# Kernel optimization log

Hardware: AMD Instinct MI355X
Metric: run time of the kernel (lower is better)

The kernel has to match this reference:

```python
import jax, jax.numpy as jnp
import numpy as np

B, L, D = 1, 2048, 2048
H, KV, HD = 32, 8, 64
REP = H // KV  # GQA repeat factor = 4


def _rope(t, cos, sin):
    # t: (B, L, nH, HD); cos/sin: (L, HD//2). Complex rotation on (even, odd) pairs.
    tr = t.reshape(*t.shape[:-1], HD // 2, 2)
    xr, xi = tr[..., 0], tr[..., 1]
    c = cos[None, :, None, :]
    s = sin[None, :, None, :]
    out_r = xr * c - xi * s
    out_i = xr * s + xi * c
    return jnp.stack([out_r, out_i], axis=-1).reshape(t.shape)


def setup_inputs() -> dict:
    key = jax.random.key(0)
    ks = jax.random.split(key, 5)
    x = jax.random.normal(ks[0], (B, L, D), jnp.float32)
    wq = jax.random.normal(ks[1], (D, H * HD), jnp.float32) * 0.02
    wk = jax.random.normal(ks[2], (D, KV * HD), jnp.float32) * 0.02
    wv = jax.random.normal(ks[3], (D, KV * HD), jnp.float32) * 0.02
    wo = jax.random.normal(ks[4], (H * HD, D), jnp.float32) * 0.02
    pos = jnp.arange(L, dtype=jnp.float32)
    inv_freq = 1.0 / (10000.0 ** (jnp.arange(0, HD, 2, dtype=jnp.float32) / HD))
    ang = pos[:, None] * inv_freq[None, :]  # (L, HD//2)
    freqs_cos = jnp.cos(ang)
    freqs_sin = jnp.sin(ang)
    # causal additive mask (L, L): 0 on/below diagonal, large negative above
    causal = jnp.arange(L)[None, :] <= jnp.arange(L)[:, None]
    mask = jnp.where(causal, 0.0, -1e9).astype(jnp.float32)
    return {"x": x, "wq": wq, "wk": wk, "wv": wv, "wo": wo,
            "freqs_cos": freqs_cos, "freqs_sin": freqs_sin, "mask": mask}


def reference(x, wq, wk, wv, wo, freqs_cos, freqs_sin, mask):
    q = (x @ wq).reshape(B, L, H, HD)
    k = (x @ wk).reshape(B, L, KV, HD)
    v = (x @ wv).reshape(B, L, KV, HD)
    q = _rope(q, freqs_cos, freqs_sin)
    k = _rope(k, freqs_cos, freqs_sin)
    # GQA: repeat_interleave kv heads
    k = jnp.repeat(k, REP, axis=2)
    v = jnp.repeat(v, REP, axis=2)
    # (B, nH, L, HD)
    q = q.transpose(0, 2, 1, 3)
    k = k.transpose(0, 2, 1, 3)
    v = v.transpose(0, 2, 1, 3)
    scores = jnp.einsum('bhqd,bhkd->bhqk', q, k) / np.float32(np.sqrt(HD))
    scores = scores + mask[None, None, :, :]
    attn = jax.nn.softmax(scores.astype(jnp.float32), axis=-1).astype(q.dtype)
    out = jnp.einsum('bhqk,bhkd->bqhd', attn, v).reshape(B, L, H * HD)
    return out @ wo
```

## Files before the change

### kernel.cpp

```cpp
#include <hip/hip_runtime.h>
#include <hip/hip_bf16.h>

#define L 2048
#define D 2048
#define NH 32
#define NKV 8
#define HD 64

typedef unsigned short u16;
typedef __attribute__((ext_vector_type(8))) short bf16x8;
typedef __attribute__((ext_vector_type(4))) short bf16x4;
typedef __attribute__((ext_vector_type(4))) float f32x4;

#define QSCALE 0.1803368801f

__device__ __forceinline__ f32x4 mfma16(bf16x4 a, bf16x4 b, f32x4 c) {
    return __builtin_amdgcn_mfma_f32_16x16x16bf16_1k(a, b, c, 0, 0, 0);
}

#define PANEL_OFF(d0, k) ((((size_t)((d0) >> 7) * 64 + ((k) >> 5)) << 12) + (((d0) & 127) << 5) + ((k) & 31))

__device__ __forceinline__ u16 f2bf(float x) {
    __hip_bfloat16 b = __float2bfloat16(x);
    return *reinterpret_cast<u16*>(&b);
}

__device__ __forceinline__ void gload_lds16(const void* g, void* l) {
    __builtin_amdgcn_global_load_lds(
        (const __attribute__((address_space(1))) unsigned int*)g,
        (__attribute__((address_space(3))) unsigned int*)l, 16, 0, 0);
}

__global__ __launch_bounds__(256) void prep_kernel(
    const float* __restrict__ x, u16* __restrict__ xb,
    const float* __restrict__ wq, const float* __restrict__ wk,
    const float* __restrict__ wv, const float* __restrict__ wo,
    u16* __restrict__ wqkvT, u16* __restrict__ woT)
{
    const int z = blockIdx.z;
    if (z == 4) {
        int i = (blockIdx.y * 64 + blockIdx.x) * 256 + threadIdx.x;
        int e = i * 4;
        int row = e >> 11, k0 = e & 2047;
        float4 v = ((const float4*)x)[i];
        ushort4 o;
        o.x = f2bf(v.x); o.y = f2bf(v.y); o.z = f2bf(v.z); o.w = f2bf(v.w);
        *(ushort4*)&xb[PANEL_OFF(row, k0)] = o;
        return;
    }
    const float* src; u16* dst; int C;
    if (z == 0)      { src = wq; dst = wqkvT;                           C = 2048; }
    else if (z == 1) { src = wk; dst = wqkvT + (size_t)2048 * 2048;     C = 512;  }
    else if (z == 2) { src = wv; dst = wqkvT + (size_t)2560 * 2048;     C = 512;  }
    else             { src = wo; dst = woT;                             C = 2048; }
    const int c0 = blockIdx.x * 32;
    if (c0 >= C) return;
    const int r0 = blockIdx.y * 32;
    __shared__ float tile[32][33];
    const int tx = threadIdx.x & 31, ty = threadIdx.x >> 5;
#pragma unroll
    for (int i = 0; i < 32; i += 8)
        tile[ty + i][tx] = src[(size_t)(r0 + ty + i) * C + c0 + tx];
    __syncthreads();
#pragma unroll
    for (int i = 0; i < 32; i += 8) {
        const int n = c0 + ty + i, k = r0 + tx;
        dst[PANEL_OFF(n, k)] = f2bf(tile[tx][ty + i]);
    }
}

#define VT_LDS 72

template <int MODE>
__global__ __launch_bounds__(256) void gemm4w_kernel(
    const u16* __restrict__ A, const u16* __restrict__ Bt, void* __restrict__ Cout,
    int N, int K, const float* __restrict__ fc, const float* __restrict__ fs,
    u16* __restrict__ vt)
{
    __shared__ __align__(16) u16 As[4][128 * 32];
    __shared__ __align__(16) u16 Bs[4][128 * 32];
    const int tid = threadIdx.x;
    const int w = tid >> 6, lane = tid & 63;

    const int nwg = (int)(gridDim.x * gridDim.y);
    int bid = (int)blockIdx.y * (int)gridDim.x + (int)blockIdx.x;
    bid = (bid & 7) * (nwg >> 3) + (bid >> 3);
    const int m0 = (bid / (int)gridDim.x) * 128, n0 = (bid % (int)gridDim.x) * 128;

    const int l15 = lane & 15, quad = lane >> 4, q8 = quad * 8;
    const int wr = (w >> 1) * 64, wc = (w & 1) * 64;
    const int l8 = lane * 8;
    const int wch = w * 1024;

    const u16* pa = A  + ((size_t)(m0 >> 7) * (K / 32) << 12);
    const u16* pb = Bt + ((size_t)(n0 >> 7) * (K / 32) << 12);

    f32x4 acc[4][4];
#pragma unroll
    for (int i = 0; i < 4; ++i)
#pragma unroll
        for (int j = 0; j < 4; ++j) acc[i][j] = (f32x4){0.f, 0.f, 0.f, 0.f};

    const int nSub = K / 32;
    const int nOut = nSub / 2;
#pragma unroll
    for (int s = 0; s < 4; ++s) {
        const size_t so = (size_t)s << 12;
        gload_lds16(pa + so + wch + l8,       &As[s][wch]);
        gload_lds16(pa + so + wch + 512 + l8, &As[s][wch + 512]);
        gload_lds16(pb + so + wch + l8,       &Bs[s][wch]);
        gload_lds16(pb + so + wch + 512 + l8, &Bs[s][wch + 512]);
    }
    for (int it = 0; it < nOut; ++it) {
        const int s0 = 2 * it, cb0 = s0 & 3, cb1 = (s0 + 1) & 3;
        asm volatile("s_waitcnt vmcnt(8)" ::: "memory");
        asm volatile("s_barrier" ::: "memory");
        bf16x8 a0[4], a1[4], b0[4], b1[4];
#pragma unroll
        for (int t = 0; t < 4; ++t) {
            a0[t] = *(const bf16x8*)&As[cb0][(wr + t * 16 + l15) * 32 + q8];
            b0[t] = *(const bf16x8*)&Bs[cb0][(wc + t * 16 + l15) * 32 + q8];
            a1[t] = *(const bf16x8*)&As[cb1][(wr + t * 16 + l15) * 32 + q8];
            b1[t] = *(const bf16x8*)&Bs[cb1][(wc + t * 16 + l15) * 32 + q8];
        }
        asm volatile("s_waitcnt lgkmcnt(0)" ::: "memory");
        asm volatile("s_barrier" ::: "memory");
        {
            const int sp0 = s0 + 4, sp1 = s0 + 5;
            const size_t k0 = (size_t)((sp0 < nSub) ? sp0 : 0) << 12;
            const size_t k1 = (size_t)((sp1 < nSub) ? sp1 : 0) << 12;
            gload_lds16(pa + k0 + wch + l8,       &As[cb0][wch]);
            gload_lds16(pa + k0 + wch + 512 + l8, &As[cb0][wch + 512]);
            gload_lds16(pb + k0 + wch + l8,       &Bs[cb0][wch]);
            gload_lds16(pb + k0 + wch + 512 + l8, &Bs[cb0][wch + 512]);
            gload_lds16(pa + k1 + wch + l8,       &As[cb1][wch]);
            gload_lds16(pa + k1 + wch + 512 + l8, &As[cb1][wch + 512]);
            gload_lds16(pb + k1 + wch + l8,       &Bs[cb1][wch]);
            gload_lds16(pb + k1 + wch + 512 + l8, &Bs[cb1][wch + 512]);
        }
#pragma unroll
        for (int i = 0; i < 4; ++i)
#pragma unroll
            for (int j = 0; j < 4; ++j) {
                acc[i][j] = __builtin_amdgcn_mfma_f32_16x16x32_bf16(a0[i], b0[j], acc[i][j], 0, 0, 0);
                acc[i][j] = __builtin_amdgcn_mfma_f32_16x16x32_bf16(a1[i], b1[j], acc[i][j], 0, 0, 0);
            }
    }

    if (MODE == 0) {
        float* C = (float*)Cout;
#pragma unroll
        for (int i = 0; i < 4; ++i)
#pragma unroll
            for (int j = 0; j < 4; ++j)
#pragma unroll
                for (int r = 0; r < 4; ++r)
                    C[(size_t)(m0 + wr + i * 16 + quad * 4 + r) * N + n0 + wc + j * 16 + l15] = acc[i][j][r];
    } else {
        __syncthreads();
        u16* O = (u16*)Cout;
        const int vc0 = n0 + wc;
        if (vc0 < 2560) {
            const float scl = (vc0 < 2048) ? QSCALE : 1.0f;
            const int odd = l15 & 1;
#pragma unroll
            for (int i = 0; i < 4; ++i)
#pragma unroll
                for (int j = 0; j < 4; ++j)
#pragma unroll
                    for (int r = 0; r < 4; ++r) {
                        const int row = m0 + wr + i * 16 + quad * 4 + r;
                        const int col = vc0 + j * 16 + l15;
                        float v = acc[i][j][r];
                        const int i2 = (j * 16 + l15) >> 1;
                        const float c = fc[row * 32 + i2], s = fs[row * 32 + i2];
                        const float p = __shfl_xor(v, 1);
                        float o = (odd ? (p * s + v * c) : (v * c - p * s)) * scl;
                        O[(size_t)row * 3072 + col] = f2bf(o);
                    }
        } else {
            u16* ws_ = (w < 2 ? (u16*)As : (u16*)Bs) + (w & 1) * (64 * VT_LDS);
#pragma unroll
            for (int i = 0; i < 4; ++i)
#pragma unroll
                for (int j = 0; j < 4; ++j)
#pragma unroll
                    for (int r = 0; r < 4; ++r)
                        ws_[(j * 16 + l15) * VT_LDS + i * 16 + quad * 4 + r] = f2bf(acc[i][j][r]);
#pragma unroll
            for (int t = 0; t < 8; ++t) {
                const int vr = t * 8 + (lane >> 3);
                const int c8 = (lane & 7) * 8;
                bf16x8 vv = *(const bf16x8*)&ws_[vr * VT_LDS + c8];
                *(bf16x8*)&vt[(size_t)(vc0 - 2560 + vr) * 2048 + m0 + wr + c8] = vv;
            }
        }
    }
}

#define ATT_STEP(CVAL, CB)                                                     \
    {                                                                          \
        gload_lds16(pk0, &Ks[(CB) ^ 1][(w * 16) * 64]);                        \
        gload_lds16(pk1, &Ks[(CB) ^ 1][(w * 16 + 8) * 64]);                    \
        gload_lds16(pv0, &Vs[(CB) ^ 1][(w * 16) * 64]);                        \
        gload_lds16(pv1, &Vs[(CB) ^ 1][(w * 16 + 8) * 64]);                    \
        pk0 += 64 * 3072; pk1 += 64 * 3072; pv0 += 64; pv1 += 64;              \
        asm volatile("s_waitcnt vmcnt(4)" ::: "memory");                       \
        asm volatile("s_barrier" ::: "memory");                                \
        const char* KB = (const char*)Ks + (CB) * 8192;                        \
        const char* VB = (const char*)Vs + (CB) * 8192;                        \
        f32x4 s[4];                                                            \
        __builtin_amdgcn_s_setprio(1);                                         \
        _Pragma("unroll")                                                      \
        for (int kt = 0; kt < 4; ++kt) {                                       \
            bf16x8 b0 = *(const bf16x8*)(KB + kt * 2048 + aK);                 \
            bf16x8 b1 = *(const bf16x8*)(KB + kt * 2048 + aK2);                \
            f32x4 t = (f32x4){0.f, 0.f, 0.f, 0.f};                             \
            t = __builtin_amdgcn_mfma_f32_16x16x32_bf16(b0, qa[0], t, 0, 0, 0);\
            t = __builtin_amdgcn_mfma_f32_16x16x32_bf16(b1, qa[1], t, 0, 0, 0);\
            s[kt] = t;                                                         \
        }                                                                      \
        __builtin_amdgcn_s_setprio(0);                                         \
        if ((CVAL) == tile) {                                                  \
            _Pragma("unroll")                                                  \
            for (int kt = 0; kt < 4; ++kt)                                     \
                _Pragma("unroll")                                              \
                for (int r = 0; r < 4; ++r)                                    \
                    if (kt * 16 + quad * 4 + r > w * 16 + l15)                 \
                        s[kt][r] = -1e30f;                                     \
        }                                                                      \
        float mx = fmaxf(fmaxf(fmaxf(s[0][0], s[0][1]), fmaxf(s[0][2], s[0][3])), \
                         fmaxf(fmaxf(s[1][0], s[1][1]), fmaxf(s[1][2], s[1][3]))); \
        mx = fmaxf(mx, fmaxf(fmaxf(fmaxf(s[2][0], s[2][1]), fmaxf(s[2][2], s[2][3])), \
                             fmaxf(fmaxf(s[3][0], s[3][1]), fmaxf(s[3][2], s[3][3])))); \
        mx = fmaxf(mx, __shfl_xor(mx, 16));                                    \
        mx = fmaxf(mx, __shfl_xor(mx, 32));                                    \
        const bool resc = !__all(mx <= m_run + 8.f);                           \
        float aL = 1.f;                                                        \
        if (resc) {                                                            \
            const float mn = fmaxf(m_run, mx);                                 \
            aL = exp2f(m_run - mn);                                            \
            m_run = mn;                                                        \
        }                                                                      \
        _Pragma("unroll")                                                      \
        for (int kt = 0; kt < 4; ++kt)                                         \
            _Pragma("unroll")                                                  \
            for (int r = 0; r < 4; ++r) s[kt][r] = exp2f(s[kt][r] - m_run);    \
        float rsum = 0.f;                                                      \
        _Pragma("unroll")                                                      \
        for (int kt = 0; kt < 4; ++kt)                                         \
            _Pragma("unroll")                                                  \
            for (int r = 0; r < 4; ++r) rsum += s[kt][r];                      \
        rsum += __shfl_xor(rsum, 16);                                          \
        rsum += __shfl_xor(rsum, 32);                                          \
        l_run = resc ? (l_run * aL + rsum) : (l_run + rsum);                   \
        bf16x4 pbf[4];                                                         \
        _Pragma("unroll")                                                      \
        for (int kt = 0; kt < 4; ++kt) {                                       \
            unsigned int lo, hi;                                               \
            asm("v_cvt_pk_bf16_f32 %0, %1, %2" : "=v"(lo) : "v"(s[kt][0]), "v"(s[kt][1])); \
            asm("v_cvt_pk_bf16_f32 %0, %1, %2" : "=v"(hi) : "v"(s[kt][2]), "v"(s[kt][3])); \
            union { unsigned int u[2]; bf16x4 v; } cv;                         \
            cv.u[0] = lo; cv.u[1] = hi;                                        \
            pbf[kt] = cv.v;                                                    \
        }                                                                      \
        if (resc) {                                                            \
            _Pragma("unroll")                                                  \
            for (int r = 0; r < 4; ++r) {                                      \
                const float aQ = __shfl(aL, (quad << 4) + (quad << 2) + r);    \
                O[0][r] *= aQ; O[1][r] *= aQ; O[2][r] *= aQ; O[3][r] *= aQ;    \
            }                                                                  \
        }                                                                      \
        __builtin_amdgcn_s_setprio(1);                                         \
        _Pragma("unroll")                                                      \
        for (int kt = 0; kt < 4; ++kt) {                                       \
            const int aVk = aV ^ (kt * 32);                                    \
            _Pragma("unroll")                                                  \
            for (int dt = 0; dt < 4; ++dt) {                                   \
                bf16x4 vf = *(const bf16x4*)(VB + dt * 2048 + aVk);            \
                O[dt] = mfma16(pbf[kt], vf, O[dt]);                            \
            }                                                                  \
        }                                                                      \
        __builtin_amdgcn_s_setprio(0);                                         \
        asm volatile("s_barrier" ::: "memory");                                \
    }

__global__ __launch_bounds__(256) void attn_mfma_kernel(
    const u16* __restrict__ qkv,
    const u16* __restrict__ vt,
    u16* __restrict__ ab)
{
    __shared__ __align__(16) u16 Ks[2][64 * 64];
    __shared__ __align__(16) u16 Vs[2][64 * 64];

    const int h = blockIdx.x;
    const int tile = (int)gridDim.y - 1 - (int)blockIdx.y;
    const int gkv = h >> 2;
    const int tid = threadIdx.x;
    const int w = tid >> 6, lane = tid & 63;
    const int l15 = lane & 15, quad = lane >> 4;
    const int q0 = tile * 64 + w * 16;

    const int srow = lane >> 3, schunk = lane & 7;
    const int r0_ = w * 16 + srow, r1_ = r0_ + 8;
    const int c0_ = (schunk ^ (r0_ & 7)) * 8, c1_ = (schunk ^ (r1_ & 7)) * 8;

    const u16* pk0 = qkv + 2048 + gkv * HD + (size_t)r0_ * 3072 + c0_;
    const u16* pk1 = qkv + 2048 + gkv * HD + (size_t)r1_ * 3072 + c1_;
    const u16* pv0 = vt + (size_t)(gkv * HD + r0_) * 2048 + c0_;
    const u16* pv1 = vt + (size_t)(gkv * HD + r1_) * 2048 + c1_;

    const int kx = l15 & 7;
    const int aK  = l15 * 128 + ((quad ^ kx) * 16);
    const int aK2 = aK ^ 64;
    const int aV  = l15 * 128 + (((quad >> 1) ^ kx) * 16) + ((quad & 1) * 8);

    bf16x8 qa[2];
    {
        const u16* qrow = qkv + (size_t)(q0 + l15) * 3072 + h * HD + quad * 8;
        qa[0] = *(const bf16x8*)(qrow);
        qa[1] = *(const bf16x8*)(qrow + 32);
    }
    f32x4 O[4];
#pragma unroll
    for (int i = 0; i < 4; ++i) O[i] = (f32x4){0.f, 0.f, 0.f, 0.f};
    float m_run = -1e30f;
    float l_run = 0.f;

    gload_lds16(pk0, &Ks[0][(w * 16) * 64]);
    gload_lds16(pk1, &Ks[0][(w * 16 + 8) * 64]);
    gload_lds16(pv0, &Vs[0][(w * 16) * 64]);
    gload_lds16(pv1, &Vs[0][(w * 16 + 8) * 64]);
    pk0 += 64 * 3072; pk1 += 64 * 3072; pv0 += 64; pv1 += 64;

    for (int c = 0; c <= tile; c += 2) {
        ATT_STEP(c, 0)
        if (c + 1 <= tile) {
            ATT_STEP(c + 1, 1)
        }
    }

#pragma unroll
    for (int r = 0; r < 4; ++r) {
        const float lq = __shfl(l_run, (quad << 4) + (quad << 2) + r);
        const float inv = 1.0f / lq;
        const int q = q0 + quad * 4 + r;
        const int pbase = ((q >> 7) << 18) + ((q & 127) << 5);
#pragma unroll
        for (int dt = 0; dt < 4; ++dt) {
            const int col = h * HD + dt * 16 + l15;
            ab[pbase + ((col >> 5) << 12) + (col & 31)] = f2bf(O[dt][r] * inv);
        }
    }
}

extern "C" void kernel_launch(void* const* d_in, const int* in_sizes, int n_in,
                              void* d_out, int out_size, void* d_ws, size_t ws_size,
                              hipStream_t stream)
{
    const float* x  = (const float*)d_in[0];
    const float* wq = (const float*)d_in[1];
    const float* wk = (const float*)d_in[2];
    const float* wv = (const float*)d_in[3];
    const float* wo = (const float*)d_in[4];
    const float* fc = (const float*)d_in[5];
    const float* fs = (const float*)d_in[6];
    float* out = (float*)d_out;

    u16* xb     = (u16*)d_ws;
    u16* wqkvT  = xb     + (size_t)2048 * 2048;
    u16* woT    = wqkvT  + (size_t)3072 * 2048;
    u16* qkv_bf = woT    + (size_t)2048 * 2048;
    u16* vt     = qkv_bf + (size_t)2048 * 3072;
    u16* ab     = vt     + (size_t)512 * 2048;

    prep_kernel<<<dim3(64, 64, 5), 256, 0, stream>>>(x, xb, wq, wk, wv, wo, wqkvT, woT);

    gemm4w_kernel<1><<<dim3(3072 / 128, 2048 / 128), 256, 0, stream>>>(
        xb, wqkvT, qkv_bf, 3072, 2048, fc, fs, vt);

    attn_mfma_kernel<<<dim3(NH, L / 64), 256, 0, stream>>>(qkv_bf, vt, ab);

    gemm4w_kernel<0><<<dim3(2048 / 128, 2048 / 128), 256, 0, stream>>>(
        ab, woT, out, 2048, 2048, nullptr, nullptr, nullptr);
}
```

Before: 244.1 us.

## Deepen GEMM LDS ring to 8 stages, split MFMA phases, widen prep transpose tiles

```diff
diff --git a/kernel.cpp b/kernel.cpp
--- a/kernel.cpp
+++ b/kernel.cpp
@@ -38,14 +38,19 @@
     u16* __restrict__ wqkvT, u16* __restrict__ woT)
 {
     const int z = blockIdx.z;
+    const int tid = threadIdx.x;
     if (z == 4) {
-        int i = (blockIdx.y * 64 + blockIdx.x) * 256 + threadIdx.x;
-        int e = i * 4;
-        int row = e >> 11, k0 = e & 2047;
-        float4 v = ((const float4*)x)[i];
-        ushort4 o;
-        o.x = f2bf(v.x); o.y = f2bf(v.y); o.z = f2bf(v.z); o.w = f2bf(v.w);
-        *(ushort4*)&xb[PANEL_OFF(row, k0)] = o;
+        const int base = (blockIdx.y * 32 + blockIdx.x) * 1024 + tid;
+#pragma unroll
+        for (int k = 0; k < 4; ++k) {
+            const int i = base + k * 256;
+            const int e = i * 4;
+            const int row = e >> 11, k0 = e & 2047;
+            float4 v = ((const float4*)x)[i];
+            ushort4 o;
+            o.x = f2bf(v.x); o.y = f2bf(v.y); o.z = f2bf(v.z); o.w = f2bf(v.w);
+            *(ushort4*)&xb[PANEL_OFF(row, k0)] = o;
+        }
         return;
     }
     const float* src; u16* dst; int C;
@@ -53,19 +58,29 @@
     else if (z == 1) { src = wk; dst = wqkvT + (size_t)2048 * 2048;     C = 512;  }
     else if (z == 2) { src = wv; dst = wqkvT + (size_t)2560 * 2048;     C = 512;  }
     else             { src = wo; dst = woT;                             C = 2048; }
-    const int c0 = blockIdx.x * 32;
+    const int c0 = blockIdx.x * 64;
     if (c0 >= C) return;
-    const int r0 = blockIdx.y * 32;
-    __shared__ float tile[32][33];
-    const int tx = threadIdx.x & 31, ty = threadIdx.x >> 5;
-#pragma unroll
-    for (int i = 0; i < 32; i += 8)
-        tile[ty + i][tx] = src[(size_t)(r0 + ty + i) * C + c0 + tx];
+    const int r0 = blockIdx.y * 64;
+    __shared__ float tile[64][65];
+    {
+        const int b4 = (tid & 15) * 4, ty = tid >> 4;
+#pragma unroll
+        for (int i = 0; i < 4; ++i) {
+            const int a = ty + i * 16;
+            float4 v = *(const float4*)&src[(size_t)(r0 + a) * C + c0 + b4];
+            tile[a][b4] = v.x; tile[a][b4 + 1] = v.y;
+            tile[a][b4 + 2] = v.z; tile[a][b4 + 3] = v.w;
+        }
+    }
     __syncthreads();
-#pragma unroll
-    for (int i = 0; i < 32; i += 8) {
-        const int n = c0 + ty + i, k = r0 + tx;
-        dst[PANEL_OFF(n, k)] = f2bf(tile[tx][ty + i]);
+    {
+        const int j = tid & 63, h16 = (tid >> 6) * 16;
+        u16 buf[16];
+#pragma unroll
+        for (int t = 0; t < 16; ++t) buf[t] = f2bf(tile[h16 + t][j]);
+        u16* d = &dst[PANEL_OFF(c0 + j, r0 + h16)];
+        *(bf16x8*)d       = *(bf16x8*)&buf[0];
+        *(bf16x8*)(d + 8) = *(bf16x8*)&buf[8];
     }
 }
 
@@ -77,8 +92,8 @@
     int N, int K, const float* __restrict__ fc, const float* __restrict__ fs,
     u16* __restrict__ vt)
 {
-    __shared__ __align__(16) u16 As[4][128 * 32];
-    __shared__ __align__(16) u16 Bs[4][128 * 32];
+    __shared__ __align__(16) u16 As[8][128 * 32];
+    __shared__ __align__(16) u16 Bs[8][128 * 32];
     const int tid = threadIdx.x;
     const int w = tid >> 6, lane = tid & 63;
 
@@ -104,47 +119,63 @@
     const int nSub = K / 32;
     const int nOut = nSub / 2;
 #pragma unroll
-    for (int s = 0; s < 4; ++s) {
+    for (int s = 0; s < 6; ++s) {
         const size_t so = (size_t)s << 12;
         gload_lds16(pa + so + wch + l8,       &As[s][wch]);
         gload_lds16(pa + so + wch + 512 + l8, &As[s][wch + 512]);
         gload_lds16(pb + so + wch + l8,       &Bs[s][wch]);
         gload_lds16(pb + so + wch + 512 + l8, &Bs[s][wch + 512]);
     }
+    int c0i = 0;
     for (int it = 0; it < nOut; ++it) {
-        const int s0 = 2 * it, cb0 = s0 & 3, cb1 = (s0 + 1) & 3;
-        asm volatile("s_waitcnt vmcnt(8)" ::: "memory");
-        asm volatile("s_barrier" ::: "memory");
-        bf16x8 a0[4], a1[4], b0[4], b1[4];
-#pragma unroll
-        for (int t = 0; t < 4; ++t) {
-            a0[t] = *(const bf16x8*)&As[cb0][(wr + t * 16 + l15) * 32 + q8];
-            b0[t] = *(const bf16x8*)&Bs[cb0][(wc + t * 16 + l15) * 32 + q8];
-            a1[t] = *(const bf16x8*)&As[cb1][(wr + t * 16 + l15) * 32 + q8];
-            b1[t] = *(const bf16x8*)&Bs[cb1][(wc + t * 16 + l15) * 32 + q8];
-        }
-        asm volatile("s_waitcnt lgkmcnt(0)" ::: "memory");
+        asm volatile("s_waitcnt vmcnt(16)" ::: "memory");
         asm volatile("s_barrier" ::: "memory");
         {
-            const int sp0 = s0 + 4, sp1 = s0 + 5;
+            const int pi0 = (c0i == 0) ? 6 : c0i - 2;
+            const int sp0 = 2 * it + 6, sp1 = 2 * it + 7;
             const size_t k0 = (size_t)((sp0 < nSub) ? sp0 : 0) << 12;
             const size_t k1 = (size_t)((sp1 < nSub) ? sp1 : 0) << 12;
-            gload_lds16(pa + k0 + wch + l8,       &As[cb0][wch]);
-            gload_lds16(pa + k0 + wch + 512 + l8, &As[cb0][wch + 512]);
-            gload_lds16(pb + k0 + wch + l8,       &Bs[cb0][wch]);
-            gload_lds16(pb + k0 + wch + 512 + l8, &Bs[cb0][wch + 512]);
-            gload_lds16(pa + k1 + wch + l8,       &As[cb1][wch]);
-            gload_lds16(pa + k1 + wch + 512 + l8, &As[cb1][wch + 512]);
-            gload_lds16(pb + k1 + wch + l8,       &Bs[cb1][wch]);
-            gload_lds16(pb + k1 + wch + 512 + l8, &Bs[cb1][wch + 512]);
-        }
-#pragma unroll
-        for (int i = 0; i < 4; ++i)
-#pragma unroll
-            for (int j = 0; j < 4; ++j) {
-                acc[i][j] = __builtin_amdgcn_mfma_f32_16x16x32_bf16(a0[i], b0[j], acc[i][j], 0, 0, 0);
-                acc[i][j] = __builtin_amdgcn_mfma_f32_16x16x32_bf16(a1[i], b1[j], acc[i][j], 0, 0, 0);
+            gload_lds16(pa + k0 + wch + l8,       &As[pi0][wch]);
+            gload_lds16(pa + k0 + wch + 512 + l8, &As[pi0][wch + 512]);
+            gload_lds16(pb + k0 + wch + l8,       &Bs[pi0][wch]);
+            gload_lds16(pb + k0 + wch + 512 + l8, &Bs[pi0][wch + 512]);
+            gload_lds16(pa + k1 + wch + l8,       &As[pi0 + 1][wch]);
+            gload_lds16(pa + k1 + wch + 512 + l8, &As[pi0 + 1][wch + 512]);
+            gload_lds16(pb + k1 + wch + l8,       &Bs[pi0 + 1][wch]);
+            gload_lds16(pb + k1 + wch + 512 + l8, &Bs[pi0 + 1][wch + 512]);
+        }
+        const int cb0 = c0i, cb1 = c0i + 1;
+        {
+            bf16x8 a0[4], b0v[4];
+#pragma unroll
+            for (int t = 0; t < 4; ++t) {
+                a0[t]  = *(const bf16x8*)&As[cb0][(wr + t * 16 + l15) * 32 + q8];
+                b0v[t] = *(const bf16x8*)&Bs[cb0][(wc + t * 16 + l15) * 32 + q8];
             }
+            __builtin_amdgcn_s_setprio(1);
+#pragma unroll
+            for (int i = 0; i < 4; ++i)
+#pragma unroll
+                for (int j = 0; j < 4; ++j)
+                    acc[i][j] = __builtin_amdgcn_mfma_f32_16x16x32_bf16(a0[i], b0v[j], acc[i][j], 0, 0, 0);
+            __builtin_amdgcn_s_setprio(0);
+        }
+        {
+            bf16x8 a1[4], b1v[4];
+#pragma unroll
+            for (int t = 0; t < 4; ++t) {
+                a1[t]  = *(const bf16x8*)&As[cb1][(wr + t * 16 + l15) * 32 + q8];
+                b1v[t] = *(const bf16x8*)&Bs[cb1][(wc + t * 16 + l15) * 32 + q8];
+            }
+            __builtin_amdgcn_s_setprio(1);
+#pragma unroll
+            for (int i = 0; i < 4; ++i)
+#pragma unroll
+                for (int j = 0; j < 4; ++j)
+                    acc[i][j] = __builtin_amdgcn_mfma_f32_16x16x32_bf16(a1[i], b1v[j], acc[i][j], 0, 0, 0);
+            __builtin_amdgcn_s_setprio(0);
+        }
+        c0i = (c0i == 6) ? 0 : c0i + 2;
     }
 
     if (MODE == 0) {
@@ -374,7 +405,7 @@
     u16* vt     = qkv_bf + (size_t)2048 * 3072;
     u16* ab     = vt     + (size_t)512 * 2048;
 
-    prep_kernel<<<dim3(64, 64, 5), 256, 0, stream>>>(x, xb, wq, wk, wv, wo, wqkvT, woT);
+    prep_kernel<<<dim3(32, 32, 5), 256, 0, stream>>>(x, xb, wq, wk, wv, wo, wqkvT, woT);
 
     gemm4w_kernel<1><<<dim3(3072 / 128, 2048 / 128), 256, 0, stream>>>(
         xb, wqkvT, qkv_bf, 3072, 2048, fc, fs, vt);
```

Measured after the change: 288.4 us. 1.18x slower.
